# Kernel tuning notes

Measured on AMD Instinct MI355X. Metric: run time of the kernel, lower is better.

Reference implementation:

```python
import jax, jax.numpy as jnp
import numpy as np


def setup_inputs() -> dict:
    key = jax.random.key(0)
    k = jax.random.split(key, 8)
    n, C, L = 16, 32, 128
    dim, out_c, n_pieces = 256, 128, 20
    x = jax.random.normal(k[0], (n, C, L), dtype=jnp.float32)
    mask = jnp.ones((n, L), dtype=jnp.float32)
    # conv1: Conv2d(2C+2, dim, 1) -> weight [dim, 2C+2]
    fan1 = 2 * C + 2
    w1 = jax.random.normal(k[1], (dim, fan1), dtype=jnp.float32) / np.sqrt(fan1)
    b1 = jnp.zeros((dim,), dtype=jnp.float32)
    # conv2: Conv2d(dim, out_c, 1) -> weight [out_c, dim]
    w2 = jax.random.normal(k[2], (out_c, dim), dtype=jnp.float32) / np.sqrt(dim)
    b2 = jnp.zeros((out_c,), dtype=jnp.float32)
    # FSPool weight: [out_c, n_pieces+1], init normal_
    pool_w = jax.random.normal(k[3], (out_c, n_pieces + 1), dtype=jnp.float32)
    return {"x": x, "mask": mask, "w1": w1, "b1": b1, "w2": w2, "b2": b2, "pool_w": pool_w}


def reference(x, mask, w1, b1, w2, b2, pool_w):
    # x: [n, C, L], mask: [n, L]
    xm = jnp.concatenate([x, mask[:, None, :]], axis=1)  # [n, C+1, L]
    c1 = xm.shape[1]
    # conv1 on concat([a_expand, b_expand], dim=1) with a 1x1 conv factors:
    # W1 @ cat(a,b) = W1a @ a + W1b @ b, avoiding the [n, 2C+2, L, L] tensor.
    ha = jnp.einsum('dc,ncl->ndl', w1[:, :c1], xm)  # [n, dim, L] (row part)
    hb = jnp.einsum('dc,ncl->ndl', w1[:, c1:], xm)  # [n, dim, L] (col part)
    h = jax.nn.relu(ha[:, :, :, None] + hb[:, :, None, :] + b1[None, :, None, None])  # [n, dim, L, L]
    y = jnp.einsum('od,ndij->noij', w2, h) + b2[None, :, None, None]  # [n, out_c, L, L]
    n, oc, L, _ = y.shape
    L2 = L * L
    y = y.reshape(n, oc, L2) / L2  # x / l / l
    # FSPool: all set sizes equal L2, so the size mask is all-ones (the -99999
    # masking and (1-mask) terms are no-ops).
    n_pieces = pool_w.shape[1] - 1
    pos = jnp.minimum(jnp.arange(L2, dtype=jnp.float32) / max(L2 - 1, 1), 1.0)  # [L2]
    idx_f = n_pieces * pos
    idx = idx_f.astype(jnp.int32)
    frac = idx_f - idx.astype(jnp.float32)
    left = pool_w[:, idx]                                  # [oc, L2]
    right = pool_w[:, jnp.minimum(idx + 1, n_pieces)]      # [oc, L2]
    w = (1.0 - frac)[None, :] * left + frac[None, :] * right  # [oc, L2]
    y_sorted = -jnp.sort(-y, axis=2)  # descending sort along set dim
    pooled = jnp.sum(y_sorted * w[None, :, :], axis=2)  # [n, oc]
    return pooled
```

## Files before the change

kernel.cpp:

```cpp
#include <hip/hip_runtime.h>
#include <hip/hip_bf16.h>


#define NB 16
#define CIN 33
#define DIM 256
#define LEN 128
#define OC 128
#define L2 16384

typedef short bf16x8 __attribute__((ext_vector_type(8)));
typedef float f32x4 __attribute__((ext_vector_type(4)));

__device__ __forceinline__ unsigned short f32_to_bf16_rne(float f) {
    unsigned u = __float_as_uint(f);
    unsigned rb = ((u >> 16) & 1u) + 0x7FFFu;
    return (unsigned short)((u + rb) >> 16);
}
__device__ __forceinline__ float bf16_to_f32(unsigned short b) {
    return __uint_as_float(((unsigned)b) << 16);
}
__device__ __forceinline__ unsigned pk_bf16(float a, float b) {
    __hip_bfloat162 p = __float22bfloat162_rn(make_float2(a, b));
    unsigned w;
    __builtin_memcpy(&w, &p, 4);
    return w;
}

__global__ __launch_bounds__(128) void kA(const float* __restrict__ x,
                                          const float* __restrict__ mask,
                                          const float* __restrict__ w1,
                                          const float* __restrict__ b1,
                                          float* __restrict__ ha,
                                          float* __restrict__ hb) {
    int d = blockIdx.x;
    int n = blockIdx.y;
    int l = threadIdx.x;
    const float* w1r = w1 + d * (2 * CIN);
    float a = 0.f, b = 0.f;
#pragma unroll
    for (int c = 0; c < CIN; ++c) {
        float xv = (c < 32) ? x[((size_t)n * 32 + c) * LEN + l] : mask[(size_t)n * LEN + l];
        a = fmaf(w1r[c], xv, a);
        b = fmaf(w1r[CIN + c], xv, b);
    }
    float hb1 = 0.5f * b1[d];
    ha[((size_t)n * DIM + d) * LEN + l] = a + hb1;
    hb[((size_t)n * DIM + d) * LEN + l] = b + hb1;
}

__global__ __launch_bounds__(256) void kW(const float* __restrict__ w2,
                                          unsigned short* __restrict__ w2hi,
                                          unsigned short* __restrict__ w2lo) {
    int idx = blockIdx.x * 256 + threadIdx.x;
    float v = w2[idx];
    unsigned short h = f32_to_bf16_rne(v);
    unsigned short l = f32_to_bf16_rne(v - bf16_to_f32(h));
    w2hi[idx] = h;
    w2lo[idx] = l;
}

#define ROWP 40
__global__ __launch_bounds__(256) void kB(const float* __restrict__ ha,
                                          const float* __restrict__ hb,
                                          const unsigned short* __restrict__ w2hi,
                                          const unsigned short* __restrict__ w2lo,
                                          const float* __restrict__ b2,
                                          unsigned short* __restrict__ y,
                                          int nbase) {
    __shared__ unsigned short Bh[128 * ROWP];
    __shared__ float ha_s[DIM];
    int i0 = blockIdx.x;
    int zloc = blockIdx.y;
    int n = nbase + zloc;
    int tid = threadIdx.x;
    int wv = tid >> 6, l = tid & 63;
    int g = l >> 4, lr = l & 15;

    if (tid < DIM) ha_s[tid] = ha[((size_t)n * DIM + tid) * LEN + i0];

    f32x4 acc[2][8];
#pragma unroll
    for (int mt = 0; mt < 2; ++mt) {
        float bv[4];
#pragma unroll
        for (int r = 0; r < 4; ++r) bv[r] = b2[(wv * 2 + mt) * 16 + g * 4 + r];
#pragma unroll
        for (int nt = 0; nt < 8; ++nt)
#pragma unroll
            for (int r = 0; r < 4; ++r) acc[mt][nt][r] = bv[r];
    }

    const float* hbN = hb + (size_t)n * DIM * LEN;
    int j = tid & 127, kh = tid >> 7;
    __syncthreads();

    for (int d0 = 0; d0 < DIM; d0 += 32) {
        {
            union { unsigned w[8]; uint4 q[2]; } pkv;
#pragma unroll
            for (int kk = 0; kk < 16; kk += 2) {
                int d = d0 + kh * 16 + kk;
                float h0 = fmaxf(ha_s[d] + hbN[(size_t)d * LEN + j], 0.f);
                float h1 = fmaxf(ha_s[d + 1] + hbN[(size_t)(d + 1) * LEN + j], 0.f);
                pkv.w[kk >> 1] = pk_bf16(h0, h1);
            }
            *(uint4*)&Bh[j * ROWP + kh * 16] = pkv.q[0];
            *(uint4*)&Bh[j * ROWP + kh * 16 + 8] = pkv.q[1];
        }
        __syncthreads();

        bf16x8 ah[2], al[2];
#pragma unroll
        for (int mt = 0; mt < 2; ++mt) {
            int row = (wv * 2 + mt) * 16 + lr;
            ah[mt] = *(const bf16x8*)&w2hi[(size_t)row * DIM + d0 + g * 8];
            al[mt] = *(const bf16x8*)&w2lo[(size_t)row * DIM + d0 + g * 8];
        }
#pragma unroll
        for (int nt = 0; nt < 8; ++nt) {
            int brow = nt * 16 + lr;
            bf16x8 bh = *(bf16x8*)&Bh[brow * ROWP + g * 8];
#pragma unroll
            for (int mt = 0; mt < 2; ++mt) {
                acc[mt][nt] = __builtin_amdgcn_mfma_f32_16x16x32_bf16(ah[mt], bh, acc[mt][nt], 0, 0, 0);
                acc[mt][nt] = __builtin_amdgcn_mfma_f32_16x16x32_bf16(al[mt], bh, acc[mt][nt], 0, 0, 0);
            }
        }
        __syncthreads();
    }

#pragma unroll
    for (int mt = 0; mt < 2; ++mt)
#pragma unroll
        for (int nt = 0; nt < 8; ++nt)
#pragma unroll
            for (int r = 0; r < 4; ++r) {
                int o = (wv * 2 + mt) * 16 + g * 4 + r;
                int col = nt * 16 + lr;
                y[((size_t)zloc * OC + o) * L2 + (size_t)i0 * LEN + col] =
                    f32_to_bf16_rne(acc[mt][nt][r]);
            }
}

__device__ __forceinline__ unsigned swz(unsigned w) { return w ^ ((w >> 2) & 0xCu); }

__global__ __launch_bounds__(1024, 8) void kC(const unsigned short* __restrict__ y,
                                              const float* __restrict__ pw,
                                              float* __restrict__ out,
                                              int nbase) {
    extern __shared__ unsigned hist[];
    int row = blockIdx.x;
    int och = row & (OC - 1);
    int n = nbase + (row >> 7);
    int t = threadIdx.x;
    int lane = t & 63, wv = t >> 6;
    const unsigned short* yr = y + (size_t)row * L2;
    const float* pwo = pw + och * 21;
    int tsw = (t & 3) << 2;

#pragma unroll
    for (int q = 0; q < 4; ++q)
        *(uint4*)&hist[t * 16 + ((q << 2) ^ tsw)] = make_uint4(0, 0, 0, 0);
    __syncthreads();

    unsigned off16[8];
    {
        union { uint4 q[2]; unsigned short u[16]; } ld;
        ld.q[0] = *(const uint4*)&yr[t * 16];
        ld.q[1] = *(const uint4*)&yr[t * 16 + 8];
#pragma unroll
        for (int e = 0; e < 16; ++e) {
            unsigned u = ld.u[e];
            unsigned k16 = u ^ ((u & 0x8000u) ? 0xFFFFu : 0x8000u);
            unsigned hi = (k16 >> 1) & 1;
            unsigned old = atomicAdd(&hist[swz(k16 >> 2)], hi ? 0x10000u : 1u);
            unsigned myoff = hi ? (old >> 16) : (old & 0xFFFFu);
            if (e & 1) off16[e >> 1] |= myoff << 16;
            else       off16[e >> 1] = myoff;
        }
    }
    __syncthreads();

    int Ti = 0;
#pragma unroll
    for (int q = 0; q < 4; ++q) {
        uint4 v4 = *(const uint4*)&hist[t * 16 + ((q << 2) ^ tsw)];
        Ti += (int)(v4.x & 0xFFFFu) + (int)(v4.x >> 16);
        Ti += (int)(v4.y & 0xFFFFu) + (int)(v4.y >> 16);
        Ti += (int)(v4.z & 0xFFFFu) + (int)(v4.z >> 16);
        Ti += (int)(v4.w & 0xFFFFu) + (int)(v4.w >> 16);
    }
    int incl = Ti;
#pragma unroll
    for (int d = 1; d < 64; d <<= 1) {
        int u2 = __shfl_up(incl, d, 64);
        if (lane >= d) incl += u2;
    }
    if (lane == 63) hist[16384 + wv] = (unsigned)incl;
    __syncthreads();
    int base = 0;
#pragma unroll
    for (int k = 0; k < 16; ++k) {
        int tw = (int)hist[16384 + k];
        base += (k < wv) ? tw : 0;
    }
    int P = base + (incl - Ti);

#pragma unroll
    for (int q = 0; q < 4; ++q) {
        unsigned* wp = &hist[t * 16 + ((q << 2) ^ tsw)];
        uint4 v4 = *(const uint4*)wp;
        unsigned r4[4] = {v4.x, v4.y, v4.z, v4.w};
#pragma unroll
        for (int c = 0; c < 4; ++c) {
            int clo = (int)(r4[c] & 0xFFFFu), chi = (int)(r4[c] >> 16);
            P += clo;
            unsigned slo = (unsigned)(L2 - P);
            P += chi;
            unsigned shi = (unsigned)(L2 - P);
            r4[c] = slo | (shi << 16);
        }
        *(uint4*)wp = make_uint4(r4[0], r4[1], r4[2], r4[3]);
    }
    __syncthreads();

    float acc = 0.f;
    {
        union { uint4 q[2]; unsigned short u[16]; } ld;
        ld.q[0] = *(const uint4*)&yr[t * 16];
        ld.q[1] = *(const uint4*)&yr[t * 16 + 8];
#pragma unroll
        for (int e = 0; e < 16; ++e) {
            unsigned u = ld.u[e];
            unsigned k16 = u ^ ((u & 0x8000u) ? 0xFFFFu : 0x8000u);
            unsigned hi = (k16 >> 1) & 1;
            unsigned w = hist[swz(k16 >> 2)];
            unsigned start = hi ? (w >> 16) : (w & 0xFFFFu);
            unsigned myoff = (e & 1) ? (off16[e >> 1] >> 16) : (off16[e >> 1] & 0xFFFFu);
            int r = (int)(start + myoff);
            float posf = fminf((float)r / 16383.0f, 1.0f);
            float idxf = 20.0f * posf;
            int idx = (int)idxf;
            float frac = idxf - (float)idx;
            int i1 = min(idx + 1, 20);
            float wvw = (1.0f - frac) * pwo[idx] + frac * pwo[i1];
            float val = __uint_as_float(((unsigned)u) << 16);
            acc = fmaf(val, wvw, acc);
        }
    }

#pragma unroll
    for (int d = 32; d >= 1; d >>= 1) acc += __shfl_xor(acc, d, 64);
    __syncthreads();
    if (lane == 0) ((float*)hist)[16384 + wv] = acc;
    __syncthreads();
    if (t == 0) {
        double tot = 0.0;
#pragma unroll
        for (int k = 0; k < 16; ++k) tot += (double)((const float*)hist)[16384 + k];
        out[(size_t)n * OC + och] = (float)(tot * (1.0 / (double)L2));
    }
}

extern "C" void kernel_launch(void* const* d_in, const int* in_sizes, int n_in,
                              void* d_out, int out_size, void* d_ws, size_t ws_size,
                              hipStream_t stream) {
    const float* x    = (const float*)d_in[0];
    const float* mask = (const float*)d_in[1];
    const float* w1   = (const float*)d_in[2];
    const float* b1   = (const float*)d_in[3];
    const float* w2   = (const float*)d_in[4];
    const float* b2   = (const float*)d_in[5];
    const float* pw   = (const float*)d_in[6];
    float* out = (float*)d_out;

    char* ws = (char*)d_ws;
    float* ha = (float*)ws;
    float* hb = ha + (size_t)NB * DIM * LEN;
    unsigned short* w2hi = (unsigned short*)(ws + (size_t)2 * NB * DIM * LEN * 4);
    unsigned short* w2lo = w2hi + (size_t)OC * DIM;
    unsigned short* y = w2lo + (size_t)OC * DIM;

    size_t used = (size_t)2 * NB * DIM * LEN * 4 + (size_t)2 * OC * DIM * 2;
    size_t perN = (size_t)OC * L2 * 2;
    int nchunk = 1;
    if (ws_size > used + perN) {
        size_t c = (ws_size - used) / perN;
        nchunk = (int)(c > NB ? NB : c);
    }

    hipLaunchKernelGGL(kA, dim3(DIM, NB), dim3(128), 0, stream, x, mask, w1, b1, ha, hb);
    hipLaunchKernelGGL(kW, dim3(OC * DIM / 256), dim3(256), 0, stream, w2, w2hi, w2lo);
    for (int base = 0; base < NB; base += nchunk) {
        int nc = nchunk < (NB - base) ? nchunk : (NB - base);
        hipLaunchKernelGGL(kB, dim3(LEN, nc), dim3(256), 0, stream, ha, hb, w2hi, w2lo, b2, y, base);
        hipLaunchKernelGGL(kC, dim3(OC * nc), dim3(1024), 65600, stream, y, pw, out, base);
    }
}
```

Measured before the change: 142.5 us.

## Replace per-element rank weighting with per-bin prefix-sum weight integration

```diff
diff --git a/kernel.cpp b/kernel.cpp
--- a/kernel.cpp
+++ b/kernel.cpp
@@ -145,6 +145,25 @@
 
 __device__ __forceinline__ unsigned swz(unsigned w) { return w ^ ((w >> 2) & 0xCu); }
 
+__device__ __forceinline__ float evalW(int R, const float* WcT, const float* pwT) {
+    if (R <= 0) return 0.f;
+    int rm1 = R - 1;
+    float posf = fminf((float)rm1 * (1.0f / 16383.0f), 1.0f);
+    int p = (int)(20.0f * posf);
+    int a = (16383 * p + 19) / 20;
+    int N = R - a;
+    long long M = (long long)N * (10LL * (a + R - 1) - 16383LL * p);
+    float dp = (p < 20) ? (pwT[p + 1] - pwT[p]) : 0.f;
+    return WcT[p] + (float)N * pwT[p] + dp * (float)((double)M * (1.0 / 16383.0));
+}
+
+__device__ __forceinline__ float binval(int bin) {
+    unsigned k0 = (unsigned)(bin << 1), k1 = k0 + 1;
+    unsigned b0 = (k0 & 0x8000u) ? (k0 ^ 0x8000u) : (k0 ^ 0xFFFFu);
+    unsigned b1 = (k1 & 0x8000u) ? (k1 ^ 0x8000u) : (k1 ^ 0xFFFFu);
+    return 0.5f * (__uint_as_float(b0 << 16) + __uint_as_float(b1 << 16));
+}
+
 __global__ __launch_bounds__(1024, 8) void kC(const unsigned short* __restrict__ y,
                                               const float* __restrict__ pw,
                                               float* __restrict__ out,
@@ -158,13 +177,14 @@
     const unsigned short* yr = y + (size_t)row * L2;
     const float* pwo = pw + och * 21;
     int tsw = (t & 3) << 2;
+    float* WcT = (float*)&hist[16384 + 16];
+    float* pwT = (float*)&hist[16384 + 40];
 
 #pragma unroll
     for (int q = 0; q < 4; ++q)
         *(uint4*)&hist[t * 16 + ((q << 2) ^ tsw)] = make_uint4(0, 0, 0, 0);
     __syncthreads();
 
-    unsigned off16[8];
     {
         union { uint4 q[2]; unsigned short u[16]; } ld;
         ld.q[0] = *(const uint4*)&yr[t * 16];
@@ -173,11 +193,28 @@
         for (int e = 0; e < 16; ++e) {
             unsigned u = ld.u[e];
             unsigned k16 = u ^ ((u & 0x8000u) ? 0xFFFFu : 0x8000u);
-            unsigned hi = (k16 >> 1) & 1;
-            unsigned old = atomicAdd(&hist[swz(k16 >> 2)], hi ? 0x10000u : 1u);
-            unsigned myoff = hi ? (old >> 16) : (old & 0xFFFFu);
-            if (e & 1) off16[e >> 1] |= myoff << 16;
-            else       off16[e >> 1] = myoff;
+            atomicAdd(&hist[swz(k16 >> 2)], ((k16 >> 1) & 1) ? 0x10000u : 1u);
+        }
+    }
+
+    if (wv == 0) {
+        int p = lane;
+        int a = (16383 * p + 19) / 20;
+        int e2 = (p >= 20) ? L2 : (16383 * (p + 1) + 19) / 20;
+        int N = e2 - a;
+        float wp0 = (p <= 20) ? pwo[p] : 0.f;
+        float wp1 = (p < 20) ? pwo[p + 1] : wp0;
+        long long M = (long long)N * (10LL * (a + e2 - 1) - 16383LL * p);
+        double ps = (double)N * (double)wp0 + (double)(wp1 - wp0) * ((double)M * (1.0 / 16383.0));
+        double s = ps;
+#pragma unroll
+        for (int d = 1; d < 64; d <<= 1) {
+            double u2 = __shfl_up(s, d, 64);
+            if (lane >= d) s += u2;
+        }
+        if (p <= 20) {
+            WcT[p] = (float)(s - ps);
+            pwT[p] = wp0;
         }
     }
     __syncthreads();
@@ -199,61 +236,46 @@
     }
     if (lane == 63) hist[16384 + wv] = (unsigned)incl;
     __syncthreads();
-    int base = 0;
+    int P = 0;
 #pragma unroll
     for (int k = 0; k < 16; ++k) {
         int tw = (int)hist[16384 + k];
-        base += (k < wv) ? tw : 0;
-    }
-    int P = base + (incl - Ti);
-
+        P += (k < wv) ? tw : 0;
+    }
+    P += (incl - Ti);
+
+    float contrib = 0.f;
+    float Wprev = evalW(L2 - P, WcT, pwT);
 #pragma unroll
     for (int q = 0; q < 4; ++q) {
-        unsigned* wp = &hist[t * 16 + ((q << 2) ^ tsw)];
-        uint4 v4 = *(const uint4*)wp;
-        unsigned r4[4] = {v4.x, v4.y, v4.z, v4.w};
-#pragma unroll
-        for (int c = 0; c < 4; ++c) {
-            int clo = (int)(r4[c] & 0xFFFFu), chi = (int)(r4[c] >> 16);
-            P += clo;
-            unsigned slo = (unsigned)(L2 - P);
-            P += chi;
-            unsigned shi = (unsigned)(L2 - P);
-            r4[c] = slo | (shi << 16);
-        }
-        *(uint4*)wp = make_uint4(r4[0], r4[1], r4[2], r4[3]);
-    }
-    __syncthreads();
-
-    float acc = 0.f;
-    {
-        union { uint4 q[2]; unsigned short u[16]; } ld;
-        ld.q[0] = *(const uint4*)&yr[t * 16];
-        ld.q[1] = *(const uint4*)&yr[t * 16 + 8];
-#pragma unroll
-        for (int e = 0; e < 16; ++e) {
-            unsigned u = ld.u[e];
-            unsigned k16 = u ^ ((u & 0x8000u) ? 0xFFFFu : 0x8000u);
-            unsigned hi = (k16 >> 1) & 1;
-            unsigned w = hist[swz(k16 >> 2)];
-            unsigned start = hi ? (w >> 16) : (w & 0xFFFFu);
-            unsigned myoff = (e & 1) ? (off16[e >> 1] >> 16) : (off16[e >> 1] & 0xFFFFu);
-            int r = (int)(start + myoff);
-            float posf = fminf((float)r / 16383.0f, 1.0f);
-            float idxf = 20.0f * posf;
-            int idx = (int)idxf;
-            float frac = idxf - (float)idx;
-            int i1 = min(idx + 1, 20);
-            float wvw = (1.0f - frac) * pwo[idx] + frac * pwo[i1];
-            float val = __uint_as_float(((unsigned)u) << 16);
-            acc = fmaf(val, wvw, acc);
-        }
-    }
-
-#pragma unroll
-    for (int d = 32; d >= 1; d >>= 1) acc += __shfl_xor(acc, d, 64);
-    __syncthreads();
-    if (lane == 0) ((float*)hist)[16384 + wv] = acc;
+        uint4 v4 = *(const uint4*)&hist[t * 16 + ((q << 2) ^ tsw)];
+        unsigned wd[4] = {v4.x, v4.y, v4.z, v4.w};
+#pragma unroll
+        for (int c4 = 0; c4 < 4; ++c4) {
+            unsigned cw = wd[c4];
+            if (cw) {
+                int binb = (t * 16 + q * 4 + c4) * 2;
+                int clo = (int)(cw & 0xFFFFu), chi = (int)(cw >> 16);
+                if (clo) {
+                    P += clo;
+                    float Wn = evalW(L2 - P, WcT, pwT);
+                    contrib = fmaf(binval(binb), Wprev - Wn, contrib);
+                    Wprev = Wn;
+                }
+                if (chi) {
+                    P += chi;
+                    float Wn = evalW(L2 - P, WcT, pwT);
+                    contrib = fmaf(binval(binb + 1), Wprev - Wn, contrib);
+                    Wprev = Wn;
+                }
+            }
+        }
+    }
+
+#pragma unroll
+    for (int d = 32; d >= 1; d >>= 1) contrib += __shfl_xor(contrib, d, 64);
+    __syncthreads();
+    if (lane == 0) ((float*)hist)[16384 + wv] = contrib;
     __syncthreads();
     if (t == 0) {
         double tot = 0.0;
@@ -295,6 +317,6 @@
     for (int base = 0; base < NB; base += nchunk) {
         int nc = nchunk < (NB - base) ? nchunk : (NB - base);
         hipLaunchKernelGGL(kB, dim3(LEN, nc), dim3(256), 0, stream, ha, hb, w2hi, w2lo, b2, y, base);
-        hipLaunchKernelGGL(kC, dim3(OC * nc), dim3(1024), 65600, stream, y, pw, out, base);
-    }
-}
+        hipLaunchKernelGGL(kC, dim3(OC * nc), dim3(1024), (16384 + 64) * 4, stream, y, pw, out, base);
+    }
+}
```

After: 151.4 us. +6.2%, slower.

## Process two rows per block in kB to reuse hb loads and W2 fragments

Applied to the files above, without the earlier changes.

```diff
diff --git a/kernel.cpp b/kernel.cpp
--- a/kernel.cpp
+++ b/kernel.cpp
@@ -68,18 +68,22 @@
                                           const float* __restrict__ b2,
                                           unsigned short* __restrict__ y,
                                           int nbase) {
-    __shared__ unsigned short Bh[128 * ROWP];
-    __shared__ float ha_s[DIM];
-    int i0 = blockIdx.x;
+    __shared__ unsigned short Bh0[128 * ROWP], Bh1[128 * ROWP];
+    __shared__ float ha_s[2 * DIM];
+    int i0 = blockIdx.x * 2;
     int zloc = blockIdx.y;
     int n = nbase + zloc;
     int tid = threadIdx.x;
     int wv = tid >> 6, l = tid & 63;
     int g = l >> 4, lr = l & 15;
 
-    if (tid < DIM) ha_s[tid] = ha[((size_t)n * DIM + tid) * LEN + i0];
-
-    f32x4 acc[2][8];
+    if (tid < DIM) {
+        const float* hp = ha + ((size_t)n * DIM + tid) * LEN + i0;
+        ha_s[tid] = hp[0];
+        ha_s[DIM + tid] = hp[1];
+    }
+
+    f32x4 acc0[2][8], acc1[2][8];
 #pragma unroll
     for (int mt = 0; mt < 2; ++mt) {
         float bv[4];
@@ -88,7 +92,10 @@
 #pragma unroll
         for (int nt = 0; nt < 8; ++nt)
 #pragma unroll
-            for (int r = 0; r < 4; ++r) acc[mt][nt][r] = bv[r];
+            for (int r = 0; r < 4; ++r) {
+                acc0[mt][nt][r] = bv[r];
+                acc1[mt][nt][r] = bv[r];
+            }
     }
 
     const float* hbN = hb + (size_t)n * DIM * LEN;
@@ -97,16 +104,21 @@
 
     for (int d0 = 0; d0 < DIM; d0 += 32) {
         {
-            union { unsigned w[8]; uint4 q[2]; } pkv;
+            union { unsigned w[8]; uint4 q[2]; } p0, p1;
 #pragma unroll
             for (int kk = 0; kk < 16; kk += 2) {
                 int d = d0 + kh * 16 + kk;
-                float h0 = fmaxf(ha_s[d] + hbN[(size_t)d * LEN + j], 0.f);
-                float h1 = fmaxf(ha_s[d + 1] + hbN[(size_t)(d + 1) * LEN + j], 0.f);
-                pkv.w[kk >> 1] = pk_bf16(h0, h1);
+                float hbv0 = hbN[(size_t)d * LEN + j];
+                float hbv1 = hbN[(size_t)(d + 1) * LEN + j];
+                p0.w[kk >> 1] = pk_bf16(fmaxf(ha_s[d] + hbv0, 0.f),
+                                        fmaxf(ha_s[d + 1] + hbv1, 0.f));
+                p1.w[kk >> 1] = pk_bf16(fmaxf(ha_s[DIM + d] + hbv0, 0.f),
+                                        fmaxf(ha_s[DIM + d + 1] + hbv1, 0.f));
             }
-            *(uint4*)&Bh[j * ROWP + kh * 16] = pkv.q[0];
-            *(uint4*)&Bh[j * ROWP + kh * 16 + 8] = pkv.q[1];
+            *(uint4*)&Bh0[j * ROWP + kh * 16] = p0.q[0];
+            *(uint4*)&Bh0[j * ROWP + kh * 16 + 8] = p0.q[1];
+            *(uint4*)&Bh1[j * ROWP + kh * 16] = p1.q[0];
+            *(uint4*)&Bh1[j * ROWP + kh * 16 + 8] = p1.q[1];
         }
         __syncthreads();
 
@@ -120,11 +132,14 @@
 #pragma unroll
         for (int nt = 0; nt < 8; ++nt) {
             int brow = nt * 16 + lr;
-            bf16x8 bh = *(bf16x8*)&Bh[brow * ROWP + g * 8];
+            bf16x8 bh0 = *(bf16x8*)&Bh0[brow * ROWP + g * 8];
+            bf16x8 bh1 = *(bf16x8*)&Bh1[brow * ROWP + g * 8];
 #pragma unroll
             for (int mt = 0; mt < 2; ++mt) {
-                acc[mt][nt] = __builtin_amdgcn_mfma_f32_16x16x32_bf16(ah[mt], bh, acc[mt][nt], 0, 0, 0);
-                acc[mt][nt] = __builtin_amdgcn_mfma_f32_16x16x32_bf16(al[mt], bh, acc[mt][nt], 0, 0, 0);
+                acc0[mt][nt] = __builtin_amdgcn_mfma_f32_16x16x32_bf16(ah[mt], bh0, acc0[mt][nt], 0, 0, 0);
+                acc0[mt][nt] = __builtin_amdgcn_mfma_f32_16x16x32_bf16(al[mt], bh0, acc0[mt][nt], 0, 0, 0);
+                acc1[mt][nt] = __builtin_amdgcn_mfma_f32_16x16x32_bf16(ah[mt], bh1, acc1[mt][nt], 0, 0, 0);
+                acc1[mt][nt] = __builtin_amdgcn_mfma_f32_16x16x32_bf16(al[mt], bh1, acc1[mt][nt], 0, 0, 0);
             }
         }
         __syncthreads();
@@ -138,8 +153,9 @@
             for (int r = 0; r < 4; ++r) {
                 int o = (wv * 2 + mt) * 16 + g * 4 + r;
                 int col = nt * 16 + lr;
-                y[((size_t)zloc * OC + o) * L2 + (size_t)i0 * LEN + col] =
-                    f32_to_bf16_rne(acc[mt][nt][r]);
+                size_t base = ((size_t)zloc * OC + o) * L2 + (size_t)i0 * LEN + col;
+                y[base] = f32_to_bf16_rne(acc0[mt][nt][r]);
+                y[base + LEN] = f32_to_bf16_rne(acc1[mt][nt][r]);
             }
 }
 
@@ -294,7 +310,7 @@
     hipLaunchKernelGGL(kW, dim3(OC * DIM / 256), dim3(256), 0, stream, w2, w2hi, w2lo);
     for (int base = 0; base < NB; base += nchunk) {
         int nc = nchunk < (NB - base) ? nchunk : (NB - base);
-        hipLaunchKernelGGL(kB, dim3(LEN, nc), dim3(256), 0, stream, ha, hb, w2hi, w2lo, b2, y, base);
+        hipLaunchKernelGGL(kB, dim3(LEN / 2, nc), dim3(256), 0, stream, ha, hb, w2hi, w2lo, b2, y, base);
         hipLaunchKernelGGL(kC, dim3(OC * nc), dim3(1024), 65600, stream, y, pw, out, base);
     }
 }
```

After: 157.8 us. 10.7% more time.
